# Kernel optimization log

Measured on AMD Instinct MI355X. Metric: run time of the kernel, lower is better.

## Reference

```python
import jax, jax.numpy as jnp
import numpy as np

V, D, H, L, T_BLOCK = 32000, 1024, 16, 4, 1024
HD = D // H
FF = 4 * D
EPS = 1e-5


def layer_norm(x, w, b):
    mu = jnp.mean(x, axis=-1, keepdims=True)
    var = jnp.mean(jnp.square(x - mu), axis=-1, keepdims=True)
    return (x - mu) * jax.lax.rsqrt(var + EPS) * w + b


def setup_inputs() -> dict:
    key = jax.random.key(0)
    ks = iter(jax.random.split(key, 32))
    s = 0.02
    inp = {
        "idx": jax.random.randint(next(ks), (4, 1024), 0, V, dtype=jnp.int32),
        "tok_emb": jax.random.normal(next(ks), (V, D), jnp.float32) * s,
        "pos_emb": jax.random.normal(next(ks), (T_BLOCK, D), jnp.float32) * s,
        "ln1_w": jnp.ones((L, D), jnp.float32),
        "ln1_b": jnp.zeros((L, D), jnp.float32),
        "wq": jax.random.normal(next(ks), (L, D, D), jnp.float32) * s,
        "wk": jax.random.normal(next(ks), (L, D, D), jnp.float32) * s,
        "wv": jax.random.normal(next(ks), (L, D, D), jnp.float32) * s,
        "wproj": jax.random.normal(next(ks), (L, D, D), jnp.float32) * s,
        "bproj": jnp.zeros((L, D), jnp.float32),
        "ln2_w": jnp.ones((L, D), jnp.float32),
        "ln2_b": jnp.zeros((L, D), jnp.float32),
        "w1": jax.random.normal(next(ks), (L, D, FF), jnp.float32) * s,
        "b1": jnp.zeros((L, FF), jnp.float32),
        "w2": jax.random.normal(next(ks), (L, FF, D), jnp.float32) * s,
        "b2": jnp.zeros((L, D), jnp.float32),
        "lnf_w": jnp.ones((D,), jnp.float32),
        "lnf_b": jnp.zeros((D,), jnp.float32),
        "wout": jax.random.normal(next(ks), (D, V), jnp.float32) * s,
        "bout": jnp.zeros((V,), jnp.float32),
    }
    return inp


def reference(idx, tok_emb, pos_emb, ln1_w, ln1_b, wq, wk, wv, wproj, bproj,
              ln2_w, ln2_b, w1, b1, w2, b2, lnf_w, lnf_b, wout, bout):
    B, T = idx.shape
    x = tok_emb[idx] + pos_emb[:T]  # (B,T,D)
    causal = jnp.tril(jnp.ones((T, T), bool))
    scale = 1.0 / jnp.sqrt(jnp.asarray(HD, x.dtype))
    for l in range(L):
        h = layer_norm(x, ln1_w[l], ln1_b[l])
        q = (h @ wq[l]).reshape(B, T, H, HD)
        k = (h @ wk[l]).reshape(B, T, H, HD)
        v = (h @ wv[l]).reshape(B, T, H, HD)
        scores = jnp.einsum('bqhd,bkhd->bhqk', q, k) * scale
        scores = jnp.where(causal, scores, -jnp.inf)
        weights = jax.nn.softmax(scores, axis=-1)
        attn = jnp.einsum('bhqk,bkhd->bqhd', weights, v).reshape(B, T, D)
        x = x + attn @ wproj[l] + bproj[l]
        h2 = layer_norm(x, ln2_w[l], ln2_b[l])
        x = x + jax.nn.relu(h2 @ w1[l] + b1[l]) @ w2[l] + b2[l]
    x = layer_norm(x, lnf_w, lnf_b)
    logits = x @ wout + bout  # (B,T,V)
    return logits
```

## Files before the change

### kernel.cpp

```cpp
#include <hip/hip_runtime.h>
#include <hip/hip_bf16.h>

#define V_  32000
#define D_  1024
#define H_  16
#define L_  4
#define T_  1024
#define B_  4
#define HD_ 64
#define FF_ 4096
#define M_  4096
#define QP_ 3072

typedef unsigned short u16;
typedef float  f32x4   __attribute__((ext_vector_type(4)));
typedef float  f32x16  __attribute__((ext_vector_type(16)));
typedef __bf16 bf16x8  __attribute__((ext_vector_type(8)));
typedef u16    us8     __attribute__((ext_vector_type(8)));

typedef __attribute__((address_space(1))) void gvoid;
typedef __attribute__((address_space(3))) void lvoid;

__device__ __forceinline__ void glds16(const void* g, void* l) {
  __builtin_amdgcn_global_load_lds((gvoid*)g, (lvoid*)l, 16, 0, 0);
}
__device__ __forceinline__ u16 f2bf(float f) {
  __hip_bfloat16 h = __float2bfloat16(f);
  return reinterpret_cast<u16&>(h);
}

__global__ __launch_bounds__(256) void embed_kernel(
    const int* __restrict__ idx, const float* __restrict__ tok,
    const float* __restrict__ pos, float* __restrict__ x)
{
  int bt = blockIdx.x;
  int t  = bt & (T_ - 1);
  int id = idx[bt];
  float4 a = ((const float4*)(tok + (size_t)id * D_))[threadIdx.x];
  float4 p = ((const float4*)(pos + (size_t)t  * D_))[threadIdx.x];
  a.x += p.x; a.y += p.y; a.z += p.z; a.w += p.w;
  ((float4*)(x + (size_t)bt * D_))[threadIdx.x] = a;
}

__global__ __launch_bounds__(256) void ln_kernel(
    const float* __restrict__ x, const float* __restrict__ w,
    const float* __restrict__ b, u16* __restrict__ out)
{
  int row = blockIdx.x;
  float4 v = ((const float4*)(x + (size_t)row * D_))[threadIdx.x];
  float s  = v.x + v.y + v.z + v.w;
  float s2 = v.x * v.x + v.y * v.y + v.z * v.z + v.w * v.w;
#pragma unroll
  for (int m = 1; m < 64; m <<= 1) { s += __shfl_xor(s, m); s2 += __shfl_xor(s2, m); }
  __shared__ float ssum[4], ssum2[4];
  int wv = threadIdx.x >> 6;
  if ((threadIdx.x & 63) == 0) { ssum[wv] = s; ssum2[wv] = s2; }
  __syncthreads();
  s  = ssum[0]  + ssum[1]  + ssum[2]  + ssum[3];
  s2 = ssum2[0] + ssum2[1] + ssum2[2] + ssum2[3];
  float mu  = s * (1.f / D_);
  float var = s2 * (1.f / D_) - mu * mu;
  float rs  = rsqrtf(var + 1e-5f);
  float4 wv4 = ((const float4*)w)[threadIdx.x];
  float4 bv4 = ((const float4*)b)[threadIdx.x];
  u16* o = out + (size_t)row * D_ + threadIdx.x * 4;
  o[0] = f2bf((v.x - mu) * rs * wv4.x + bv4.x);
  o[1] = f2bf((v.y - mu) * rs * wv4.y + bv4.y);
  o[2] = f2bf((v.z - mu) * rs * wv4.z + bv4.z);
  o[3] = f2bf((v.w - mu) * rs * wv4.w + bv4.w);
}

__global__ __launch_bounds__(256) void transpose_convert(
    const float* __restrict__ in, u16* __restrict__ out, int R, int C,
    size_t inStride, size_t outStride)
{
  __shared__ float tile[32][33];
  in  += (size_t)blockIdx.z * inStride;
  out += (size_t)blockIdx.z * outStride;
  int c  = blockIdx.x * 32 + threadIdx.x;
  int r0 = blockIdx.y * 32;
#pragma unroll
  for (int j = 0; j < 4; j++)
    tile[threadIdx.y + 8 * j][threadIdx.x] =
        in[(size_t)(r0 + threadIdx.y + 8 * j) * C + c];
  __syncthreads();
  int rr = r0 + threadIdx.x;
  int cb = blockIdx.x * 32;
#pragma unroll
  for (int j = 0; j < 4; j++)
    out[(size_t)(cb + threadIdx.y + 8 * j) * R + rr] =
        f2bf(tile[threadIdx.x][threadIdx.y + 8 * j]);
}

template<int EPI>
__global__ __launch_bounds__(256) void gemm_bt(
    const u16* __restrict__ A, const u16* __restrict__ Bt,
    const float* __restrict__ bias, const float* __restrict__ resid,
    void* __restrict__ Cout, int M, int N, int K)
{
  __shared__ u16 As[128 * 32];
  __shared__ u16 Bs[128 * 32];
  const int tid = threadIdx.x;
  const int m0 = blockIdx.x * 128;
  const int n0 = blockIdx.y * 128;
  const int w = tid >> 6, lane = tid & 63, lg = lane >> 4, lr = lane & 15;
  const int wr = w >> 1, wc = w & 1;
  f32x4 acc[4][4] = {};
  const int srow = tid >> 2;
  const int scol = (tid & 3) << 3;
  const u16* ap = A  + (size_t)(m0 + srow) * K + scol;
  const u16* bp = Bt + (size_t)(n0 + srow) * K + scol;
  u16* alds  = &As[tid * 8];
  u16* alds2 = &As[2048 + tid * 8];
  u16* blds  = &Bs[tid * 8];
  u16* blds2 = &Bs[2048 + tid * 8];
  for (int k0 = 0; k0 < K; k0 += 32) {
    __syncthreads();
    glds16(ap + k0,                  alds);
    glds16(ap + (size_t)64 * K + k0, alds2);
    glds16(bp + k0,                  blds);
    glds16(bp + (size_t)64 * K + k0, blds2);
    __syncthreads();
    bf16x8 af[4], bfr[4];
#pragma unroll
    for (int i = 0; i < 4; i++)
      af[i] = *(const bf16x8*)&As[(wr * 64 + i * 16 + lr) * 32 + lg * 8];
#pragma unroll
    for (int j = 0; j < 4; j++)
      bfr[j] = *(const bf16x8*)&Bs[(wc * 64 + j * 16 + lr) * 32 + lg * 8];
#pragma unroll
    for (int i = 0; i < 4; i++)
#pragma unroll
      for (int j = 0; j < 4; j++)
        acc[i][j] = __builtin_amdgcn_mfma_f32_16x16x32_bf16(af[i], bfr[j], acc[i][j], 0, 0, 0);
  }
#pragma unroll
  for (int i = 0; i < 4; i++) {
#pragma unroll
    for (int j = 0; j < 4; j++) {
      int col = n0 + wc * 64 + j * 16 + lr;
      float bv = bias ? bias[col] : 0.f;
#pragma unroll
      for (int r = 0; r < 4; r++) {
        int row = m0 + wr * 64 + i * 16 + lg * 4 + r;
        float val = acc[i][j][r] + bv;
        size_t o = (size_t)row * N + col;
        if (EPI == 0)      ((u16*)Cout)[o]   = f2bf(val);
        else if (EPI == 1) ((u16*)Cout)[o]   = f2bf(val > 0.f ? val : 0.f);
        else if (EPI == 2) ((float*)Cout)[o] = resid[o] + val;
        else               ((float*)Cout)[o] = val;
      }
    }
  }
}

#define BAR() __builtin_amdgcn_s_barrier()
#define VMC(n) asm volatile("s_waitcnt vmcnt(" #n ")" ::: "memory")
#define LGKMC(n) do { asm volatile("s_waitcnt lgkmcnt(" #n ")" ::: "memory"); \
                      __builtin_amdgcn_sched_barrier(0); } while (0)

#define CLUSTER(AF, BV, MS) do { \
  __builtin_amdgcn_s_setprio(1); \
  _Pragma("unroll") for (int mq_ = 0; mq_ < 2; ++mq_) \
  _Pragma("unroll") for (int nq_ = 0; nq_ < 2; ++nq_) \
  _Pragma("unroll") for (int kq_ = 0; kq_ < 2; ++kq_) \
    acc[(MS)+mq_][nq_] = __builtin_amdgcn_mfma_f32_32x32x16_bf16( \
        AF[mq_][kq_], BV[nq_][kq_], acc[(MS)+mq_][nq_], 0, 0, 0); \
  __builtin_amdgcn_s_setprio(0); \
} while (0)

template<int EPI>
__global__ __launch_bounds__(512, 2) void gemm256(
    const u16* __restrict__ A, const u16* __restrict__ Bt,
    const float* __restrict__ bias, void* __restrict__ Cout, int N, int K)
{
  extern __shared__ char smem[];
  const int tid = threadIdx.x;
  const int nwg = gridDim.x;
  const int orig = blockIdx.x;
  const int qq = nwg >> 3, rr = nwg & 7, xcd = orig & 7, lid = orig >> 3;
  const int swz = (xcd < rr ? xcd * (qq + 1) : rr * (qq + 1) + (xcd - rr) * qq) + lid;
  const int m0 = (swz & 15) << 8;
  const int n0 = (swz >> 4) << 8;
  const int NT = K >> 6;

  const int wid = tid >> 6, lane = tid & 63;
  const int wr = wid >> 2, wc = wid & 3;
  const int l31 = lane & 31, lh = lane >> 5;
  const int gsw = (lane & 7) ^ ((lane >> 3) & 3);
  const int srow = tid >> 3, sslot = tid & 7;
  const int sg = (srow & 7) ^ ((srow >> 3) & 3);
  const int scol = ((sslot ^ sg) << 3);
  const u16* Ag = A  + (size_t)(m0 + srow) * K + scol;
  const u16* Bg = Bt + (size_t)(n0 + srow) * K + scol;
  char* ldst = smem + tid * 16;

  auto stA = [&](int bb, int kt, int h) {
    const u16* g = Ag + (size_t)(h << 7) * K + (kt << 6);
    char* l = ldst + bb * 65536 + h * 16384;
    glds16(g, l);
    glds16(g + ((size_t)K << 6), l + 8192);
  };
  auto stB = [&](int bb, int kt, int h) {
    const u16* g = Bg + (size_t)(h << 7) * K + (kt << 6);
    char* l = ldst + bb * 65536 + 32768 + h * 16384;
    glds16(g, l);
    glds16(g + ((size_t)K << 6), l + 8192);
  };
  auto ldA = [&](int bb, int mf, int ks) {
    return *(const bf16x8*)(smem + bb * 65536 +
        ((wr * 128 + mf * 32 + l31) << 7) + (((ks * 2 + lh) ^ gsw) << 4));
  };
  auto ldB = [&](int bb, int nf, int ks) {
    return *(const bf16x8*)(smem + bb * 65536 + 32768 +
        ((wc * 64 + nf * 32 + l31) << 7) + (((ks * 2 + lh) ^ gsw) << 4));
  };

  f32x16 acc[4][2] = {};
  bf16x8 afA[2][2], afB[2][2], bfvA[2][2], bfvB[2][2];

  stA(0, 0, 0); stA(0, 0, 1); stB(0, 0, 0); stB(0, 0, 1);
  VMC(0); BAR();

  for (int t = 0; t < NT; ++t) {
    const int bb = t & 1;
    if (t + 1 < NT) {
      stA(bb ^ 1, t + 1, 0); stA(bb ^ 1, t + 1, 1);
      stB(bb ^ 1, t + 1, 0); stB(bb ^ 1, t + 1, 1);
    }
#pragma unroll
    for (int i = 0; i < 2; i++) {
      afA[i][0]  = ldA(bb, i, 0);     afA[i][1]  = ldA(bb, i, 1);
      bfvA[i][0] = ldB(bb, i, 0);     bfvA[i][1] = ldB(bb, i, 1);
    }
#pragma unroll
    for (int i = 0; i < 2; i++) { afB[i][0] = ldA(bb, 2 + i, 0); afB[i][1] = ldA(bb, 2 + i, 1); }
    LGKMC(4);
    CLUSTER(afA, bfvA, 0);
#pragma unroll
    for (int i = 0; i < 2; i++) { bfvB[i][0] = ldB(bb, i, 2); bfvB[i][1] = ldB(bb, i, 3); }
#pragma unroll
    for (int i = 0; i < 2; i++) { afA[i][0] = ldA(bb, i, 2); afA[i][1] = ldA(bb, i, 3); }
    LGKMC(8);
    CLUSTER(afB, bfvA, 2);
#pragma unroll
    for (int i = 0; i < 2; i++) { afB[i][0] = ldA(bb, 2 + i, 2); afB[i][1] = ldA(bb, 2 + i, 3); }
    LGKMC(4);
    CLUSTER(afA, bfvB, 0);
    LGKMC(0);
    CLUSTER(afB, bfvB, 2);
    VMC(0); BAR();
  }

#pragma unroll
  for (int nf = 0; nf < 2; ++nf) {
    const int col = n0 + wc * 64 + nf * 32 + l31;
    const float bv = bias ? bias[col] : 0.f;
#pragma unroll
    for (int mf = 0; mf < 4; ++mf) {
#pragma unroll
      for (int v = 0; v < 16; ++v) {
        const int row = m0 + wr * 128 + mf * 32 + (v & 3) + 8 * (v >> 2) + 4 * lh;
        float val = acc[mf][nf][v] + bv;
        size_t o = (size_t)row * N + col;
        if (EPI == 0)      ((u16*)Cout)[o]   = f2bf(val);
        else if (EPI == 1) ((u16*)Cout)[o]   = f2bf(val > 0.f ? val : 0.f);
        else               ((float*)Cout)[o] = val;
      }
    }
  }
}

__global__ __launch_bounds__(512) void attn_kernel(
    const u16* __restrict__ qkv, u16* __restrict__ o)
{
  __shared__ u16 Ks[64][72];
  __shared__ u16 Vt[64][72];
  __shared__ u16 Ps[8][16][72];
  const int qt = blockIdx.x;
  const int bh = blockIdx.y;
  const int b = bh >> 4, h = bh & 15;
  const int tid = threadIdx.x;
  const int w = tid >> 6, lane = tid & 63, lg = lane >> 4, lr = lane & 15;
  const int q0 = qt * 128;
  const size_t qbase = ((size_t)b * T_) * QP_ + h * HD_;
  const size_t obase = ((size_t)b * T_) * D_ + h * HD_;
  const u16* qb = qkv + qbase;
  const u16* kb = qkv + qbase + D_;
  const u16* vb = qkv + qbase + 2 * D_;
  bf16x8 qf[2];
  const int qrow = q0 + w * 16 + lr;
#pragma unroll
  for (int ks = 0; ks < 2; ks++)
    qf[ks] = *(const bf16x8*)&qb[(size_t)qrow * QP_ + ks * 32 + lg * 8];
  f32x4 oacc[4] = {};
  float mrun[4] = {-1e30f, -1e30f, -1e30f, -1e30f};
  float lrun[4] = {0.f, 0.f, 0.f, 0.f};
  const int srow = tid >> 3;
  const int scol = (tid & 7) << 3;
  const int ktmax = 2 * qt + 1;
  us8 kv = *(const us8*)&kb[(size_t)srow * QP_ + scol];
  us8 vv = *(const us8*)&vb[(size_t)srow * QP_ + scol];
  for (int kt = 0; kt <= ktmax; kt++) {
    __syncthreads();
    *(us8*)&Ks[srow][scol] = kv;
#pragma unroll
    for (int jj = 0; jj < 8; jj++) Vt[scol + jj][srow] = vv[jj];
    __syncthreads();
    if (kt < ktmax) {
      kv = *(const us8*)&kb[(size_t)((kt + 1) * 64 + srow) * QP_ + scol];
      vv = *(const us8*)&vb[(size_t)((kt + 1) * 64 + srow) * QP_ + scol];
    }
    f32x4 s[4] = {};
#pragma unroll
    for (int ks = 0; ks < 2; ks++)
#pragma unroll
      for (int j = 0; j < 4; j++) {
        bf16x8 kf = *(const bf16x8*)&Ks[j * 16 + lr][ks * 32 + lg * 8];
        s[j] = __builtin_amdgcn_mfma_f32_16x16x32_bf16(qf[ks], kf, s[j], 0, 0, 0);
      }
#pragma unroll
    for (int j = 0; j < 4; j++) {
      int key = kt * 64 + j * 16 + lr;
#pragma unroll
      for (int r = 0; r < 4; r++) {
        int qr = q0 + w * 16 + lg * 4 + r;
        s[j][r] = (key <= qr) ? s[j][r] * 0.125f : -1e30f;
      }
    }
    float al[4];
#pragma unroll
    for (int r = 0; r < 4; r++) {
      float t0 = fmaxf(fmaxf(s[0][r], s[1][r]), fmaxf(s[2][r], s[3][r]));
#pragma unroll
      for (int m = 1; m < 16; m <<= 1) t0 = fmaxf(t0, __shfl_xor(t0, m));
      float mnew = fmaxf(mrun[r], t0);
      al[r] = __expf(mrun[r] - mnew);
      mrun[r] = mnew;
    }
#pragma unroll
    for (int j = 0; j < 4; j++)
#pragma unroll
      for (int r = 0; r < 4; r++)
        s[j][r] = __expf(s[j][r] - mrun[r]);
#pragma unroll
    for (int r = 0; r < 4; r++) {
      float rs = s[0][r] + s[1][r] + s[2][r] + s[3][r];
#pragma unroll
      for (int m = 1; m < 16; m <<= 1) rs += __shfl_xor(rs, m);
      lrun[r] = lrun[r] * al[r] + rs;
#pragma unroll
      for (int jd = 0; jd < 4; jd++) oacc[jd][r] *= al[r];
    }
#pragma unroll
    for (int j = 0; j < 4; j++)
#pragma unroll
      for (int r = 0; r < 4; r++)
        Ps[w][lg * 4 + r][j * 16 + lr] = f2bf(s[j][r]);
    asm volatile("s_waitcnt lgkmcnt(0)" ::: "memory");
    __builtin_amdgcn_sched_barrier(0);
#pragma unroll
    for (int ks = 0; ks < 2; ks++) {
      bf16x8 pf = *(const bf16x8*)&Ps[w][lr][ks * 32 + lg * 8];
#pragma unroll
      for (int jd = 0; jd < 4; jd++) {
        bf16x8 vf = *(const bf16x8*)&Vt[jd * 16 + lr][ks * 32 + lg * 8];
        oacc[jd] = __builtin_amdgcn_mfma_f32_16x16x32_bf16(pf, vf, oacc[jd], 0, 0, 0);
      }
    }
  }
#pragma unroll
  for (int jd = 0; jd < 4; jd++)
#pragma unroll
    for (int r = 0; r < 4; r++) {
      int row = q0 + w * 16 + lg * 4 + r;
      o[obase + (size_t)row * D_ + jd * 16 + lr] = f2bf(oacc[jd][r] / lrun[r]);
    }
}

extern "C" void kernel_launch(void* const* d_in, const int* in_sizes, int n_in,
                              void* d_out, int out_size, void* d_ws, size_t ws_size,
                              hipStream_t stream)
{
  const int*   idx   = (const int*)  d_in[0];
  const float* tok   = (const float*)d_in[1];
  const float* pos   = (const float*)d_in[2];
  const float* ln1w  = (const float*)d_in[3];
  const float* ln1b  = (const float*)d_in[4];
  const float* wq    = (const float*)d_in[5];
  const float* wk    = (const float*)d_in[6];
  const float* wvw   = (const float*)d_in[7];
  const float* wproj = (const float*)d_in[8];
  const float* bproj = (const float*)d_in[9];
  const float* ln2w  = (const float*)d_in[10];
  const float* ln2b  = (const float*)d_in[11];
  const float* w1    = (const float*)d_in[12];
  const float* b1    = (const float*)d_in[13];
  const float* w2    = (const float*)d_in[14];
  const float* b2    = (const float*)d_in[15];
  const float* lnfw  = (const float*)d_in[16];
  const float* lnfb  = (const float*)d_in[17];
  const float* wout  = (const float*)d_in[18];
  const float* bout  = (const float*)d_in[19];

  hipFuncSetAttribute(reinterpret_cast<const void*>(&gemm256<0>),
                      hipFuncAttributeMaxDynamicSharedMemorySize, 131072);
  hipFuncSetAttribute(reinterpret_cast<const void*>(&gemm256<1>),
                      hipFuncAttributeMaxDynamicSharedMemorySize, 131072);
  hipFuncSetAttribute(reinterpret_cast<const void*>(&gemm256<3>),
                      hipFuncAttributeMaxDynamicSharedMemorySize, 131072);

  char* ws = (char*)d_ws;
  size_t off = 0;
  auto alloc = [&](size_t bytes) {
    void* p = ws + off;
    off += (bytes + 255) & ~(size_t)255;
    return p;
  };
  u16* wqkvT  = (u16*)alloc((size_t)L_ * 3 * D_ * D_ * 2);
  u16* wprojT = (u16*)alloc((size_t)L_ * D_ * D_ * 2);
  u16* w1T    = (u16*)alloc((size_t)L_ * D_ * FF_ * 2);
  u16* w2T    = (u16*)alloc((size_t)L_ * D_ * FF_ * 2);
  u16* woutT  = (u16*)alloc((size_t)D_ * V_ * 2);
  float* x    = (float*)alloc((size_t)M_ * D_ * 4);
  u16* hbuf   = (u16*)alloc((size_t)M_ * D_ * 2);
  u16* qkvbuf = (u16*)alloc((size_t)M_ * QP_ * 2);
  u16* abuf   = (u16*)alloc((size_t)M_ * D_ * 2);
  u16* f1buf  = (u16*)alloc((size_t)M_ * FF_ * 2);

  dim3 tb(32, 8);
  const size_t DD = (size_t)D_ * D_, DF = (size_t)D_ * FF_;
  transpose_convert<<<dim3(D_ / 32, D_ / 32, L_), tb, 0, stream>>>(wq,    wqkvT,          D_,  D_, DD, 3 * DD);
  transpose_convert<<<dim3(D_ / 32, D_ / 32, L_), tb, 0, stream>>>(wk,    wqkvT + DD,     D_,  D_, DD, 3 * DD);
  transpose_convert<<<dim3(D_ / 32, D_ / 32, L_), tb, 0, stream>>>(wvw,   wqkvT + 2 * DD, D_,  D_, DD, 3 * DD);
  transpose_convert<<<dim3(D_ / 32, D_ / 32, L_), tb, 0, stream>>>(wproj, wprojT,         D_,  D_, DD, DD);
  transpose_convert<<<dim3(FF_ / 32, D_ / 32, L_), tb, 0, stream>>>(w1,   w1T,            D_,  FF_, DF, DF);
  transpose_convert<<<dim3(D_ / 32, FF_ / 32, L_), tb, 0, stream>>>(w2,   w2T,            FF_, D_, DF, DF);
  transpose_convert<<<dim3(V_ / 32, D_ / 32, 1),  tb, 0, stream>>>(wout,  woutT,          D_,  V_, 0, 0);

  embed_kernel<<<M_, 256, 0, stream>>>(idx, tok, pos, x);

  dim3 gD(M_ / 128, D_ / 128);
  for (int l = 0; l < L_; l++) {
    size_t wo = (size_t)l * DD;
    size_t fo = (size_t)l * DF;
    ln_kernel<<<M_, 256, 0, stream>>>(x, ln1w + l * D_, ln1b + l * D_, hbuf);
    gemm256<0><<<dim3(16 * (QP_ / 256)), 512, 131072, stream>>>(
        hbuf, wqkvT + (size_t)l * 3 * DD, nullptr, qkvbuf, QP_, D_);
    attn_kernel<<<dim3(T_ / 128, B_ * H_), 512, 0, stream>>>(qkvbuf, abuf);
    gemm_bt<2><<<gD, 256, 0, stream>>>(abuf, wprojT + wo, bproj + l * D_, x, x, M_, D_, D_);
    ln_kernel<<<M_, 256, 0, stream>>>(x, ln2w + l * D_, ln2b + l * D_, hbuf);
    gemm256<1><<<dim3(16 * (FF_ / 256)), 512, 131072, stream>>>(
        hbuf, w1T + fo, b1 + l * FF_, f1buf, FF_, D_);
    gemm_bt<2><<<gD, 256, 0, stream>>>(f1buf, w2T + fo, b2 + l * D_, x, x, M_, D_, FF_);
  }
  ln_kernel<<<M_, 256, 0, stream>>>(x, lnfw, lnfb, hbuf);
  gemm256<3><<<dim3(16 * (V_ / 256)), 512, 131072, stream>>>(
      hbuf, woutT, bout, d_out, V_, D_);
}
```

Baseline: 1.643 ms.

## Pre-transpose V and double-buffer K/V via direct global-to-LDS loads in attention

Adds a small kernel that writes V transposed per batch-head into a separate buffer, so the attention kernel no longer does the scalar transpose into shared memory. The attention kernel now double-buffers K and V tiles with global_load_lds in an XOR-swizzled, unpadded layout, prefetching the next tile while the current one is computed. This removes register staging and bank-conflicted LDS stores. The cost is an extra kernel launch per layer plus the write and read of the transposed V buffer.

```diff
diff --git a/kernel.cpp b/kernel.cpp
--- a/kernel.cpp
+++ b/kernel.cpp
@@ -90,6 +90,31 @@
   for (int j = 0; j < 4; j++)
     out[(size_t)(cb + threadIdx.y + 8 * j) * R + rr] =
         f2bf(tile[threadIdx.x][threadIdx.y + 8 * j]);
+}
+
+__global__ __launch_bounds__(256) void vtrans_kernel(
+    const u16* __restrict__ qkv, u16* __restrict__ vtb)
+{
+  __shared__ u16 tile[64][72];
+  int tt = blockIdx.x, bh = blockIdx.y;
+  int b = bh >> 4, h = bh & 15;
+  const u16* src = qkv + ((size_t)(b * T_ + tt * 64)) * QP_ + 2 * D_ + h * HD_;
+#pragma unroll
+  for (int it = 0; it < 2; it++) {
+    int u = it * 256 + threadIdx.x;
+    int r = u >> 3, c = (u & 7) << 3;
+    *(us8*)&tile[r][c] = *(const us8*)&src[(size_t)r * QP_ + c];
+  }
+  __syncthreads();
+#pragma unroll
+  for (int it = 0; it < 2; it++) {
+    int u = it * 256 + threadIdx.x;
+    int d = u >> 3, t8 = (u & 7) << 3;
+    us8 v;
+#pragma unroll
+    for (int j = 0; j < 8; j++) v[j] = tile[t8 + j][d];
+    *(us8*)&vtb[((size_t)bh * HD_ + d) * T_ + tt * 64 + t8] = v;
+  }
 }
 
 template<int EPI>
@@ -272,10 +297,11 @@
 }
 
 __global__ __launch_bounds__(512) void attn_kernel(
-    const u16* __restrict__ qkv, u16* __restrict__ o)
-{
-  __shared__ u16 Ks[64][72];
-  __shared__ u16 Vt[64][72];
+    const u16* __restrict__ qkv, const u16* __restrict__ vtb,
+    u16* __restrict__ o)
+{
+  __shared__ u16 Ks[2][64][64];
+  __shared__ u16 Vs[2][64][64];
   __shared__ u16 Ps[8][16][72];
   const int qt = blockIdx.x;
   const int bh = blockIdx.y;
@@ -287,7 +313,7 @@
   const size_t obase = ((size_t)b * T_) * D_ + h * HD_;
   const u16* qb = qkv + qbase;
   const u16* kb = qkv + qbase + D_;
-  const u16* vb = qkv + qbase + 2 * D_;
+  const u16* vtbh = vtb + (size_t)bh * HD_ * T_;
   bf16x8 qf[2];
   const int qrow = q0 + w * 16 + lr;
 #pragma unroll
@@ -296,29 +322,38 @@
   f32x4 oacc[4] = {};
   float mrun[4] = {-1e30f, -1e30f, -1e30f, -1e30f};
   float lrun[4] = {0.f, 0.f, 0.f, 0.f};
-  const int srow = tid >> 3;
-  const int scol = (tid & 7) << 3;
+  const int srow = tid >> 3, sslot = tid & 7;
+  const int sg = (srow & 7) ^ ((srow >> 3) & 3);
+  const int scol = (sslot ^ sg) << 3;
+  u16* kdst = &Ks[0][0][0] + tid * 8;
+  u16* vdst = &Vs[0][0][0] + tid * 8;
+  auto stage = [&](int kt, int bb) {
+    glds16(kb + (size_t)(kt * 64 + srow) * QP_ + scol, kdst + bb * 4096);
+    glds16(vtbh + (size_t)srow * T_ + kt * 64 + scol, vdst + bb * 4096);
+  };
+  auto ldK = [&](int bb, int j, int ks) {
+    int r = j * 16 + lr;
+    int g = (r & 7) ^ ((r >> 3) & 3);
+    return *(const bf16x8*)&Ks[bb][r][((ks * 4 + lg) ^ g) << 3];
+  };
+  auto ldV = [&](int bb, int jd, int ks) {
+    int r = jd * 16 + lr;
+    int g = (r & 7) ^ ((r >> 3) & 3);
+    return *(const bf16x8*)&Vs[bb][r][((ks * 4 + lg) ^ g) << 3];
+  };
+
   const int ktmax = 2 * qt + 1;
-  us8 kv = *(const us8*)&kb[(size_t)srow * QP_ + scol];
-  us8 vv = *(const us8*)&vb[(size_t)srow * QP_ + scol];
+  stage(0, 0);
+  VMC(0); BAR();
   for (int kt = 0; kt <= ktmax; kt++) {
-    __syncthreads();
-    *(us8*)&Ks[srow][scol] = kv;
-#pragma unroll
-    for (int jj = 0; jj < 8; jj++) Vt[scol + jj][srow] = vv[jj];
-    __syncthreads();
-    if (kt < ktmax) {
-      kv = *(const us8*)&kb[(size_t)((kt + 1) * 64 + srow) * QP_ + scol];
-      vv = *(const us8*)&vb[(size_t)((kt + 1) * 64 + srow) * QP_ + scol];
-    }
+    const int bb = kt & 1;
+    if (kt < ktmax) stage(kt + 1, bb ^ 1);
     f32x4 s[4] = {};
 #pragma unroll
     for (int ks = 0; ks < 2; ks++)
 #pragma unroll
-      for (int j = 0; j < 4; j++) {
-        bf16x8 kf = *(const bf16x8*)&Ks[j * 16 + lr][ks * 32 + lg * 8];
-        s[j] = __builtin_amdgcn_mfma_f32_16x16x32_bf16(qf[ks], kf, s[j], 0, 0, 0);
-      }
+      for (int j = 0; j < 4; j++)
+        s[j] = __builtin_amdgcn_mfma_f32_16x16x32_bf16(qf[ks], ldK(bb, j, ks), s[j], 0, 0, 0);
 #pragma unroll
     for (int j = 0; j < 4; j++) {
       int key = kt * 64 + j * 16 + lr;
@@ -363,11 +398,10 @@
     for (int ks = 0; ks < 2; ks++) {
       bf16x8 pf = *(const bf16x8*)&Ps[w][lr][ks * 32 + lg * 8];
 #pragma unroll
-      for (int jd = 0; jd < 4; jd++) {
-        bf16x8 vf = *(const bf16x8*)&Vt[jd * 16 + lr][ks * 32 + lg * 8];
-        oacc[jd] = __builtin_amdgcn_mfma_f32_16x16x32_bf16(pf, vf, oacc[jd], 0, 0, 0);
-      }
-    }
+      for (int jd = 0; jd < 4; jd++)
+        oacc[jd] = __builtin_amdgcn_mfma_f32_16x16x32_bf16(pf, ldV(bb, jd, ks), oacc[jd], 0, 0, 0);
+    }
+    VMC(0); BAR();
   }
 #pragma unroll
   for (int jd = 0; jd < 4; jd++)
@@ -425,6 +459,7 @@
   float* x    = (float*)alloc((size_t)M_ * D_ * 4);
   u16* hbuf   = (u16*)alloc((size_t)M_ * D_ * 2);
   u16* qkvbuf = (u16*)alloc((size_t)M_ * QP_ * 2);
+  u16* vtb    = (u16*)alloc((size_t)B_ * H_ * HD_ * T_ * 2);
   u16* abuf   = (u16*)alloc((size_t)M_ * D_ * 2);
   u16* f1buf  = (u16*)alloc((size_t)M_ * FF_ * 2);
 
@@ -447,7 +482,8 @@
     ln_kernel<<<M_, 256, 0, stream>>>(x, ln1w + l * D_, ln1b + l * D_, hbuf);
     gemm256<0><<<dim3(16 * (QP_ / 256)), 512, 131072, stream>>>(
         hbuf, wqkvT + (size_t)l * 3 * DD, nullptr, qkvbuf, QP_, D_);
-    attn_kernel<<<dim3(T_ / 128, B_ * H_), 512, 0, stream>>>(qkvbuf, abuf);
+    vtrans_kernel<<<dim3(T_ / 64, B_ * H_), 256, 0, stream>>>(qkvbuf, vtb);
+    attn_kernel<<<dim3(T_ / 128, B_ * H_), 512, 0, stream>>>(qkvbuf, vtb, abuf);
     gemm_bt<2><<<gD, 256, 0, stream>>>(abuf, wprojT + wo, bproj + l * D_, x, x, M_, D_, D_);
     ln_kernel<<<M_, 256, 0, stream>>>(x, ln2w + l * D_, ln2b + l * D_, hbuf);
     gemm256<1><<<dim3(16 * (FF_ / 256)), 512, 131072, stream>>>(
```

New measurement: 1.634 ms. Within noise of the previous version (-0.6%).
